# Performance work log

Hardware: AMD Instinct MI355X
Metric: run time of the kernel (lower is better)

## Reference

```python
import jax, jax.numpy as jnp
from jax import lax
import numpy as np

B, T, C_IN, H, W = 2, 4, 128, 64, 64
D_MODEL, N_Q, N_POINTS, PATCH, N_LAYERS = 256, 300, 8, 3, 6


def _sine_pos(Hh, Ww, d, temperature=10000.0):
    # mask is all-False, so cumsum of ones -> arange(1..H)/H * 2pi
    two_pi = 2.0 * np.pi
    yn = (jnp.arange(1, Hh + 1, dtype=jnp.float32) / (Hh + 1e-6)) * two_pi
    xn = (jnp.arange(1, Ww + 1, dtype=jnp.float32) / (Ww + 1e-6)) * two_pi
    q = d // 4
    i = jnp.arange(q, dtype=jnp.float32)
    dim_t = temperature ** (2.0 * jnp.floor(i / 2.0) / q)
    py = yn[:, None] / dim_t
    px = xn[:, None] / dim_t
    py = jnp.stack([jnp.sin(py), jnp.cos(py)], axis=-1).reshape(Hh, 2 * q)
    px = jnp.stack([jnp.sin(px), jnp.cos(px)], axis=-1).reshape(Ww, 2 * q)
    pos = jnp.concatenate([
        jnp.broadcast_to(py[:, None, :], (Hh, Ww, 2 * q)),
        jnp.broadcast_to(px[None, :, :], (Hh, Ww, 2 * q)),
    ], axis=-1)
    return jnp.transpose(pos, (2, 0, 1))  # [d,H,W]


def _sample_scale(fmap, ref, ps):
    # fmap [B,C,h,w]; ref [B,nQ,nP,2] in [0,1]. Bilinear grid_sample,
    # padding_mode='border', align_corners=True -> direct gather (no replication).
    Bc, C, h, w = fmap.shape
    half = (ps - 1) / 2.0
    off = jnp.linspace(-half, half, ps, dtype=jnp.float32)
    oy, ox = jnp.meshgrid(off, off, indexing='ij')  # [ps,ps]
    gx = ref[..., 0, None, None] * 2.0 - 1.0 + ox * (2.0 / w)  # [B,nQ,nP,ps,ps]
    gy = ref[..., 1, None, None] * 2.0 - 1.0 + oy * (2.0 / h)
    x = jnp.clip((gx + 1.0) * 0.5 * (w - 1), 0.0, w - 1.0)
    y = jnp.clip((gy + 1.0) * 0.5 * (h - 1), 0.0, h - 1.0)
    x0 = jnp.floor(x); y0 = jnp.floor(y)
    wx = x - x0; wy = y - y0
    x0i = x0.astype(jnp.int32); y0i = y0.astype(jnp.int32)
    x1i = jnp.minimum(x0i + 1, w - 1); y1i = jnp.minimum(y0i + 1, h - 1)

    def per_b(fb, y0b, x0b, y1b, x1b, wxb, wyb):
        v00 = fb[:, y0b, x0b]  # [C,nQ,nP,ps,ps]
        v01 = fb[:, y0b, x1b]
        v10 = fb[:, y1b, x0b]
        v11 = fb[:, y1b, x1b]
        return (v00 * (1 - wxb) * (1 - wyb) + v01 * wxb * (1 - wyb)
                + v10 * (1 - wxb) * wyb + v11 * wxb * wyb)

    out = jax.vmap(per_b)(fmap, y0i, x0i, y1i, x1i, wx, wy)  # [B,C,nQ,nP,ps,ps]
    return jnp.transpose(out, (0, 2, 3, 4, 5, 1))  # [B,nQ,nP,ps,ps,C]


def reference(feat, pred_boxes_init, w_tf, b_tf, w_in, b_in, w_lat, b_lat, w_sm, b_sm,
              q_embed, q_pos, Wq, bq, Wo, bo, Wp1, bp1, Wp2, bp2,
              w_r1, b_r1, w_r2, b_r2, w_b1, b_b1, w_b2, b_b2, w_cls, b_cls):
    Bb, Tt, Cin, Hh, Ww = feat.shape
    d = w_in.shape[0]
    nP = w_r2.shape[0] // 2
    ps = int(round((Wp1.shape[-1] // d) ** 0.5))
    # temporal fuse: Conv3d kernel (3,1,1), padding (1,0,0)
    x = lax.conv_general_dilated(jnp.transpose(feat, (0, 2, 1, 3, 4)), w_tf,
                                 (1, 1, 1), [(1, 1), (0, 0), (0, 0)],
                                 dimension_numbers=('NCDHW', 'OIDHW', 'NCDHW'))
    x = x + b_tf[None, :, None, None, None]
    x = x.mean(axis=2)  # [B,Cin,H,W]
    x = jnp.einsum('bchw,dc->bdhw', x, w_in) + b_in[None, :, None, None]
    x = x + _sine_pos(Hh, Ww, d)[None]
    # FPN over scales {1,2,4}: avg_pool -> 1x1 lateral -> 3x3 smooth
    feats = []
    for i, s in enumerate((1, 2, 4)):
        xi = x if s == 1 else x.reshape(Bb, d, Hh // s, s, Ww // s, s).mean(axis=(3, 5))
        xi = jnp.einsum('bchw,oc->bohw', xi, w_lat[i]) + b_lat[i][None, :, None, None]
        xi = lax.conv_general_dilated(xi, w_sm[i], (1, 1), [(1, 1), (1, 1)],
                                      dimension_numbers=('NCHW', 'OIHW', 'NCHW'))
        xi = xi + b_sm[i][None, :, None, None]
        feats.append(xi)
    nQ = q_embed.shape[0]
    queries = jnp.broadcast_to((q_embed + q_pos)[None], (Bb, nQ, d))
    boxes = pred_boxes_init
    inv_sqrt_d = 1.0 / float(np.sqrt(d))
    for l in range(Wq.shape[0]):
        h1 = jax.nn.relu(jnp.einsum('bqd,od->bqo', queries, w_r1) + b_r1)
        ro = jnp.tanh(jnp.einsum('bqd,od->bqo', h1, w_r2) + b_r2)
        ro = ro.reshape(Bb, nQ, nP, 2) * 0.5
        ref = jnp.clip(boxes[:, :, None, :2] + ro, 0.0, 1.0)
        sampled = jnp.concatenate([_sample_scale(f, ref, ps) for f in feats], axis=2)
        sampled = sampled[:, :, :nP]  # truncate multi-scale concat back to nP
        flat = sampled.reshape(Bb, nQ, nP, ps * ps * d)
        pv = jax.nn.relu(jnp.einsum('bqpi,oi->bqpo', flat, Wp1[l]) + bp1[l])
        pv = jnp.einsum('bqpd,od->bqpo', pv, Wp2[l]) + bp2[l]
        kv = pv.mean(axis=2)  # [B,nP_q,d] -> [B,nQ,d]
        q = jnp.einsum('bqd,od->bqo', queries, Wq[l]) + bq[l]
        attn = jax.nn.softmax(jnp.einsum('bqd,bkd->bqk', q, kv) * inv_sqrt_d, axis=-1)
        out = jnp.einsum('bqk,bkd->bqd', attn, kv)
        queries = queries + (jnp.einsum('bqd,od->bqo', out, Wo[l]) + bo[l])
        hb = jax.nn.relu(jnp.einsum('bqd,od->bqo', queries, w_b1) + b_b1)
        delta = jax.nn.sigmoid(jnp.einsum('bqd,od->bqo', hb, w_b2) + b_b2)
        boxes = jnp.clip(boxes + 0.1 * jnp.tanh(delta - 0.5), 0.0, 1.0)
    logits = (jnp.einsum('bqd,od->bqo', queries, w_cls) + b_cls)[..., 0]
    return logits, boxes


def setup_inputs() -> dict:
    key = jax.random.key(0)
    keys = iter(jax.random.split(key, 48))

    def nrm(shape, s=0.02):
        return jax.random.normal(next(keys), shape, dtype=jnp.float32) * s

    inp = {
        'feat': jax.random.normal(next(keys), (B, T, C_IN, H, W), dtype=jnp.float32),
        'pred_boxes_init': jax.random.uniform(next(keys), (B, N_Q, 4), dtype=jnp.float32),
        'w_tf': nrm((C_IN, C_IN, 3, 1, 1)), 'b_tf': jnp.zeros((C_IN,), jnp.float32),
        'w_in': nrm((D_MODEL, C_IN)), 'b_in': jnp.zeros((D_MODEL,), jnp.float32),
        'w_lat': nrm((3, D_MODEL, D_MODEL)), 'b_lat': jnp.zeros((3, D_MODEL), jnp.float32),
        'w_sm': nrm((3, D_MODEL, D_MODEL, 3, 3)), 'b_sm': jnp.zeros((3, D_MODEL), jnp.float32),
        'q_embed': nrm((N_Q, D_MODEL), 1.0), 'q_pos': nrm((N_Q, D_MODEL), 1.0),
        'Wq': nrm((N_LAYERS, D_MODEL, D_MODEL)), 'bq': jnp.zeros((N_LAYERS, D_MODEL), jnp.float32),
        'Wo': nrm((N_LAYERS, D_MODEL, D_MODEL)), 'bo': jnp.zeros((N_LAYERS, D_MODEL), jnp.float32),
        'Wp1': nrm((N_LAYERS, D_MODEL, PATCH * PATCH * D_MODEL)), 'bp1': jnp.zeros((N_LAYERS, D_MODEL), jnp.float32),
        'Wp2': nrm((N_LAYERS, D_MODEL, D_MODEL)), 'bp2': jnp.zeros((N_LAYERS, D_MODEL), jnp.float32),
        'w_r1': nrm((D_MODEL, D_MODEL)), 'b_r1': jnp.zeros((D_MODEL,), jnp.float32),
        'w_r2': nrm((2 * N_POINTS, D_MODEL)), 'b_r2': jnp.zeros((2 * N_POINTS,), jnp.float32),
        'w_b1': nrm((D_MODEL, D_MODEL)), 'b_b1': jnp.zeros((D_MODEL,), jnp.float32),
        'w_b2': nrm((4, D_MODEL)), 'b_b2': jnp.zeros((4,), jnp.float32),
        'w_cls': nrm((1, D_MODEL)), 'b_cls': jnp.zeros((1,), jnp.float32),
    }
    return inp
```

## Files before the change

### kernel.cpp

```cpp
#include <hip/hip_runtime.h>
#include <hip/hip_bf16.h>
#include <math.h>

#define BB 2
#define TT 4
#define CIN 128
#define DM 256
#define NQ 300
#define NP 8
#define PS 3
#define NL 6
#define HW 4096
#define KP 2304

typedef __attribute__((ext_vector_type(8))) short short8;
typedef __attribute__((ext_vector_type(4))) short short4_t;
typedef __attribute__((ext_vector_type(4))) float f32x4;
typedef unsigned short ushort_t;

static __device__ __forceinline__ ushort_t f2bf(float f) {
  __hip_bfloat16 h = __float2bfloat16(f);
  return *reinterpret_cast<ushort_t*>(&h);
}
static __device__ __forceinline__ float bf2f(ushort_t u) {
  return __uint_as_float(((unsigned)u) << 16);
}

__global__ void k_prep(const float* __restrict__ w_in, const float* __restrict__ w_lat,
                       const float* __restrict__ Wo, const float* __restrict__ w_b1,
                       const float* __restrict__ w_r1, const float* __restrict__ Wp1,
                       ushort_t* __restrict__ win_bf, ushort_t* __restrict__ wlat_bf,
                       ushort_t* __restrict__ wo_bf, ushort_t* __restrict__ wb1_bf,
                       ushort_t* __restrict__ wr1_bf, ushort_t* __restrict__ wp1_bf,
                       const float* __restrict__ w_tf, ushort_t* __restrict__ tct,
                       const float* __restrict__ w_sm, ushort_t* __restrict__ wsm_bf,
                       const float* __restrict__ Wp2, const float* __restrict__ Wq,
                       ushort_t* __restrict__ wp2t, ushort_t* __restrict__ wqT,
                       const float* __restrict__ bq, const float* __restrict__ bp2,
                       const float* __restrict__ bo,
                       float* __restrict__ bqt, float* __restrict__ bfuse,
                       uint4* __restrict__ x2p_zero,
                       const float* __restrict__ b_tf, const float* __restrict__ b_in,
                       float* __restrict__ bias_comb,
                       const float* __restrict__ qe, const float* __restrict__ qp,
                       const float* __restrict__ pb, float* __restrict__ queries,
                       ushort_t* __restrict__ qbf, float* __restrict__ boxes) {
  __shared__ float bt[128];
  int b = blockIdx.x, t = threadIdx.x;
  if (b < 4064) {
    int i = b * 256 + t;
    const float* s; ushort_t* d; int base;
    if (i < 8192)         { s = w_in;  d = win_bf;  base = 0; }
    else if (i < 24576)   { s = w_lat; d = wlat_bf; base = 8192; }
    else if (i < 122880)  { s = Wo;    d = wo_bf;   base = 24576; }
    else if (i < 139264)  { s = w_b1;  d = wb1_bf;  base = 122880; }
    else if (i < 155648)  { s = w_r1;  d = wr1_bf;  base = 139264; }
    else                  { s = Wp1;   d = wp1_bf;  base = 155648; }
    int j = i - base;
    float4 v = ((const float4*)s)[j];
    d[j * 4 + 0] = f2bf(v.x);
    d[j * 4 + 1] = f2bf(v.y);
    d[j * 4 + 2] = f2bf(v.z);
    d[j * 4 + 3] = f2bf(v.w);
  } else if (b < 4320) {
    int i = (b - 4064) * 256 + t;
    int k = i >> 7, c = i & 127;
    int u = k >> 7, ci = k & 127;
    const float* wp = w_tf + ((size_t)(c * 128 + ci)) * 3;
    float w0 = wp[0], w1 = wp[1], w2 = wp[2];
    float coef = (u == 0) ? (w0 + w1) : (u == 3) ? (w1 + w2) : (w0 + w1 + w2);
    tct[(size_t)k * 128 + c] = f2bf(0.25f * coef);
  } else if (b < 6624) {
    int i = (b - 4320) * 256 + t;
    int n = i / KP;
    int r = i - n * KP;
    int tp = r >> 8, c = r & 255;
    wsm_bf[i] = f2bf(w_sm[((size_t)(n * 256 + c)) * 9 + tp]);
  } else if (b < 9696) {
    int i = (b - 6624) * 256 + t;
    if (i < 393216) {
      int l = i >> 16, r = i & 65535;
      int d = r >> 8, o = r & 255;
      wp2t[i] = f2bf(Wp2[((size_t)(l * 256 + o)) * 256 + d]);
    } else {
      int j = i - 393216;
      int l = j >> 16, r = j & 65535;
      int c = r >> 8, o = r & 255;
      wqT[j] = f2bf(Wq[((size_t)(l * 256 + o)) * 256 + c]);
    }
  } else if (b < 9708) {
    int i = (b - 9696) * 256 + t;
    if (i < 1536) {
      int l = i >> 8, d = i & 255;
      float a = 0.f;
      for (int o = 0; o < 256; ++o)
        a += bq[l * 256 + o] * Wp2[((size_t)(l * 256 + o)) * 256 + d];
      bqt[i] = a;
    } else {
      int j = i - 1536;
      int l = j >> 8, o2 = j & 255;
      float a = bo[l * 256 + o2];
      for (int o = 0; o < 256; ++o)
        a += bp2[l * 256 + o] * Wo[((size_t)(l * 256 + o2)) * 256 + o];
      bfuse[j] = a;
    }
  } else if (b < 10797) {
    int j = (b - 9708) * 256 + t;
    if (j < 278784) x2p_zero[j] = make_uint4(0u, 0u, 0u, 0u);
  } else if (b < 10798) {
    int d = t;
    if (d < 128) bt[d] = b_tf[d];
    __syncthreads();
    float a = b_in[d];
    for (int c = 0; c < 128; ++c) a += w_in[d * 128 + c] * bt[c];
    bias_comb[d] = a;
  } else {
    int i = (b - 10798) * 256 + t;
    if (i < BB * NQ * DM) {
      int rd = i % (NQ * DM);
      float v = qe[rd] + qp[rd];
      queries[i] = v;
      qbf[i] = f2bf(v);
    }
    if (i < BB * NQ * 4) boxes[i] = pb[i];
  }
}

__global__ __launch_bounds__(256) void k_wcompose(const ushort_t* __restrict__ wp2t,
                                                  const ushort_t* __restrict__ wqT,
                                                  const ushort_t* __restrict__ wo_bf,
                                                  ushort_t* __restrict__ wqt,
                                                  ushort_t* __restrict__ wfuse) {
  __shared__ ushort_t As[64 * 36];
  __shared__ ushort_t Bs[64 * 36];
  int z = blockIdx.z, l = z % 6;
  const ushort_t* A;
  const ushort_t* W;
  ushort_t* C;
  if (z < 6) { A = wp2t + l * 65536; W = wqT + l * 65536; C = wqt + l * 65536; }
  else       { A = wo_bf + l * 65536; W = wp2t + l * 65536; C = wfuse + l * 65536; }
  int tid = threadIdx.x;
  int bm = blockIdx.x * 64, bn = blockIdx.y * 64;
  int w = tid >> 6, lane = tid & 63;
  int wm = (w & 1) * 32, wn = (w >> 1) * 32;
  int q = lane >> 4, ml = lane & 15;
  f32x4 acc[2][2] = {};
  int srow = tid >> 2, scol = (tid & 3) * 8;
  const ushort_t* Ag = A + (size_t)(bm + srow) * 256 + scol;
  const ushort_t* Wg = W + (size_t)(bn + srow) * 256 + scol;
  for (int k0 = 0; k0 < 256; k0 += 32) {
    short8 av = *(const short8*)(Ag + k0);
    short8 wv = *(const short8*)(Wg + k0);
    *(short8*)(As + srow * 36 + scol) = av;
    *(short8*)(Bs + srow * 36 + scol) = wv;
    __syncthreads();
    short8 a0 = *(const short8*)(As + (wm + ml) * 36 + q * 8);
    short8 a1 = *(const short8*)(As + (wm + 16 + ml) * 36 + q * 8);
    short8 b0 = *(const short8*)(Bs + (wn + ml) * 36 + q * 8);
    short8 b1 = *(const short8*)(Bs + (wn + 16 + ml) * 36 + q * 8);
    acc[0][0] = __builtin_amdgcn_mfma_f32_16x16x32_bf16(a0, b0, acc[0][0], 0, 0, 0);
    acc[0][1] = __builtin_amdgcn_mfma_f32_16x16x32_bf16(a0, b1, acc[0][1], 0, 0, 0);
    acc[1][0] = __builtin_amdgcn_mfma_f32_16x16x32_bf16(a1, b0, acc[1][0], 0, 0, 0);
    acc[1][1] = __builtin_amdgcn_mfma_f32_16x16x32_bf16(a1, b1, acc[1][1], 0, 0, 0);
    __syncthreads();
  }
#pragma unroll
  for (int i = 0; i < 2; ++i)
#pragma unroll
    for (int j = 0; j < 2; ++j) {
      int cn = bn + wn + j * 16 + ml;
#pragma unroll
      for (int r = 0; r < 4; ++r) {
        int rm = bm + wm + i * 16 + q * 4 + r;
        C[(size_t)rm * 256 + cn] = f2bf(acc[i][j][r]);
      }
    }
}

__global__ __launch_bounds__(256) void k_tr(const float* __restrict__ feat,
                                            ushort_t* __restrict__ featT) {
  __shared__ float ldsF[64][65];
  int tid = threadIdx.x;
  int gs = blockIdx.x;
  int b = gs >> 6;
  int s0 = (gs & 63) * 64;
  int k0 = blockIdx.y * 64;
  int kk = tid >> 2, sc0 = (tid & 3) * 16;
  {
    int k = k0 + kk;
    int u = k >> 7, ci = k & 127;
    const float* src = feat + (((size_t)(b * 4 + u) * 128 + ci) << 12) + s0 + sc0;
#pragma unroll
    for (int j = 0; j < 4; ++j) {
      float4 v = *(const float4*)(src + j * 4);
      ldsF[kk][sc0 + j * 4 + 0] = v.x;
      ldsF[kk][sc0 + j * 4 + 1] = v.y;
      ldsF[kk][sc0 + j * 4 + 2] = v.z;
      ldsF[kk][sc0 + j * 4 + 3] = v.w;
    }
  }
  __syncthreads();
#pragma unroll
  for (int p = 0; p < 2; ++p) {
    int idx = p * 256 + tid;
    int s_l = idx >> 3, kc = (idx & 7) * 8;
    short8 v;
#pragma unroll
    for (int j = 0; j < 8; ++j) v[j] = (short)f2bf(ldsF[kc + j][s_l]);
    *(short8*)(featT + (size_t)(b * 4096 + s0 + s_l) * 512 + k0 + kc) = v;
  }
}

__global__ __launch_bounds__(256) void k_feat2(const ushort_t* __restrict__ featT,
                                               const ushort_t* __restrict__ wcomb,
                                               const float* __restrict__ biasc,
                                               ushort_t* __restrict__ xcl) {
  __shared__ ushort_t As[32 * 36];
  __shared__ ushort_t Bs[64 * 36];
  __shared__ float dimt_s[256];
  int tid = threadIdx.x;
  {
    int dd = tid & 127;
    int ii = dd >> 1;
    dimt_s[tid] = powf(10000.0f, (2.0f * (float)(ii >> 1)) / 64.0f);
  }
  int bm = blockIdx.x * 32, bn = blockIdx.y * 64;
  int w = tid >> 6, lane = tid & 63;
  int wm = (w & 1) * 16, wn = (w >> 1) * 32;
  int q = lane >> 4, ml = lane & 15;
  int sra = tid >> 3, sca = (tid & 7) * 4;
  int srb = tid >> 2, scb = (tid & 3) * 8;
  const ushort_t* Ag = featT + (size_t)(bm + sra) * 512 + sca;
  const ushort_t* Wg = wcomb + (size_t)(bn + srb) * 512 + scb;
  f32x4 acc[2] = {};
  short4_t av = *(const short4_t*)Ag;
  short8 wv = *(const short8*)Wg;
  for (int k0 = 0; k0 < 512; k0 += 32) {
    *(short4_t*)(As + sra * 36 + sca) = av;
    *(short8*)(Bs + srb * 36 + scb) = wv;
    __syncthreads();
    if (k0 + 32 < 512) {
      av = *(const short4_t*)(Ag + k0 + 32);
      wv = *(const short8*)(Wg + k0 + 32);
    }
    short8 a = *(const short8*)(As + (wm + ml) * 36 + q * 8);
    short8 b0 = *(const short8*)(Bs + (wn + ml) * 36 + q * 8);
    short8 b1 = *(const short8*)(Bs + (wn + 16 + ml) * 36 + q * 8);
    acc[0] = __builtin_amdgcn_mfma_f32_16x16x32_bf16(a, b0, acc[0], 0, 0, 0);
    acc[1] = __builtin_amdgcn_mfma_f32_16x16x32_bf16(a, b1, acc[1], 0, 0, 0);
    __syncthreads();
  }
  const float FKT = 6.28318530717958647692f / 64.000001f;
#pragma unroll
  for (int j = 0; j < 2; ++j) {
    int cn = bn + wn + j * 16 + ml;
    float dimt = dimt_s[cn];
    float bC = biasc[cn];
    bool isx = cn >= 128;
    bool isc = cn & 1;
#pragma unroll
    for (int r = 0; r < 4; ++r) {
      int rm = bm + wm + q * 4 + r;
      int s = rm & 4095;
      int y = s >> 6, x = s & 63;
      float ang = (float)((isx ? x : y) + 1) * FKT / dimt;
      float pos = isc ? cosf(ang) : sinf(ang);
      xcl[(size_t)rm * 256 + cn] = f2bf(acc[j][r] + bC + pos);
    }
  }
}

template <int ACT, int OUTMODE, int MG>
__global__ __launch_bounds__(256) void k_gemm_bf16(const ushort_t* __restrict__ A,
                                                   const ushort_t* __restrict__ W,
                                                   const float* __restrict__ bias,
                                                   const float* __restrict__ res,
                                                   float* __restrict__ Cf,
                                                   ushort_t* __restrict__ Cb,
                                                   int M, int N, int K,
                                                   const ushort_t* __restrict__ W2,
                                                   const float* __restrict__ bias2,
                                                   const ushort_t* __restrict__ W3,
                                                   const float* __restrict__ bias3) {
  __shared__ ushort_t As[64 * 36];
  __shared__ ushort_t Bs[64 * 36];
  int tid = threadIdx.x;
  int bm = blockIdx.x * 64, bn = blockIdx.y * 64;
  int w = tid >> 6, lane = tid & 63;
  int wm = (w & 1) * 32, wn = (w >> 1) * 32;
  int q = lane >> 4, ml = lane & 15;
  f32x4 acc[2][2] = {};
  int srow = tid >> 2, scol = (tid & 3) * 8;
  int ga = bm + srow;
  if (MG) ga = min(ga, M - 1);
  const ushort_t* Ag = A + (size_t)ga * K + scol;
  const ushort_t* Wg;
  if (OUTMODE == 7) {
    int seg = bn >> 8;
    const ushort_t* Wb = (seg == 0) ? W : ((seg == 1) ? W2 : W3);
    Wg = Wb + (size_t)((bn & 255) + srow) * K + scol;
  } else if (OUTMODE == 4) {
    const ushort_t* Wb = (bn < 256) ? W : W2;
    Wg = Wb + (size_t)((bn & 255) + srow) * K + scol;
  } else {
    Wg = W + (size_t)(bn + srow) * K + scol;
  }
  for (int k0 = 0; k0 < K; k0 += 32) {
    short8 av = *(const short8*)(Ag + k0);
    short8 wv = *(const short8*)(Wg + k0);
    *(short8*)(As + srow * 36 + scol) = av;
    *(short8*)(Bs + srow * 36 + scol) = wv;
    __syncthreads();
    short8 a0 = *(const short8*)(As + (wm + ml) * 36 + q * 8);
    short8 a1 = *(const short8*)(As + (wm + 16 + ml) * 36 + q * 8);
    short8 b0 = *(const short8*)(Bs + (wn + ml) * 36 + q * 8);
    short8 b1 = *(const short8*)(Bs + (wn + 16 + ml) * 36 + q * 8);
    acc[0][0] = __builtin_amdgcn_mfma_f32_16x16x32_bf16(a0, b0, acc[0][0], 0, 0, 0);
    acc[0][1] = __builtin_amdgcn_mfma_f32_16x16x32_bf16(a0, b1, acc[0][1], 0, 0, 0);
    acc[1][0] = __builtin_amdgcn_mfma_f32_16x16x32_bf16(a1, b0, acc[1][0], 0, 0, 0);
    acc[1][1] = __builtin_amdgcn_mfma_f32_16x16x32_bf16(a1, b1, acc[1][1], 0, 0, 0);
    __syncthreads();
  }
#pragma unroll
  for (int i = 0; i < 2; ++i) {
#pragma unroll
    for (int j = 0; j < 2; ++j) {
      int cn = bn + wn + j * 16 + ml;
      float bsv;
      if (OUTMODE == 7) {
        int seg = cn >> 8;
        bsv = ((seg == 0) ? bias : ((seg == 1) ? bias2 : bias3))[cn & 255];
      } else if (OUTMODE == 4) {
        bsv = ((cn < 256) ? bias : bias2)[cn & 255];
      } else {
        bsv = bias ? bias[cn] : 0.f;
      }
#pragma unroll
      for (int r = 0; r < 4; ++r) {
        int rm = bm + wm + i * 16 + q * 4 + r;
        if (MG && rm >= M) continue;
        float v = acc[i][j][r] + bsv;
        if (OUTMODE == 0) {
          if (ACT == 1) v = fmaxf(v, 0.f);
          Cf[(size_t)rm * N + cn] = v;
        } else if (OUTMODE == 1) {
          int b = rm >> 12, rem = rm & 4095;
          int y = rem >> 6, xx = rem & 63;
          Cb[(((size_t)(b * 66 + y + 1)) * 66 + xx + 1) * 256 + cn] = f2bf(v);
        } else if (OUTMODE == 2) {
          v += res[(size_t)rm * N + cn];
          Cf[(size_t)rm * N + cn] = v;
          Cb[(size_t)rm * N + cn] = f2bf(v);
        } else if (OUTMODE == 4) {
          if (cn < 256) Cf[(size_t)rm * 256 + cn] = fmaxf(v, 0.f);
          else Cb[(size_t)rm * 256 + (cn & 255)] = f2bf(v);
        } else if (OUTMODE == 6) {
          Cb[(size_t)rm * N + cn] = f2bf(v);
        } else if (OUTMODE == 7) {
          if (cn < 256) Cf[(size_t)rm * 256 + cn] = fmaxf(v, 0.f);
          else if (cn < 512) ((float*)Cb)[(size_t)rm * 256 + (cn & 255)] = fmaxf(v, 0.f);
          else ((ushort_t*)res)[(size_t)rm * 256 + (cn & 255)] = f2bf(v);
        }
      }
    }
  }
}

__global__ __launch_bounds__(256) void k_wp1_split(const ushort_t* __restrict__ A,
                                                   const ushort_t* __restrict__ W,
                                                   ushort_t* __restrict__ part) {
  __shared__ ushort_t As[64 * 36];
  __shared__ ushort_t Bs[64 * 36];
  int tid = threadIdx.x;
  int bm = blockIdx.x * 64, bn = blockIdx.y * 64;
  int kz = blockIdx.z * 768;
  int w = tid >> 6, lane = tid & 63;
  int wm = (w & 1) * 32, wn = (w >> 1) * 32;
  int q = lane >> 4, ml = lane & 15;
  int srow = tid >> 2, scol = (tid & 3) * 8;
  const ushort_t* Ag = A + (size_t)(bm + srow) * KP + kz + scol;
  const ushort_t* Wg = W + (size_t)(bn + srow) * KP + kz + scol;
  f32x4 acc[2][2] = {};
  short8 av = *(const short8*)(Ag);
  short8 wv = *(const short8*)(Wg);
  for (int k0 = 0; k0 < 768; k0 += 32) {
    *(short8*)(As + srow * 36 + scol) = av;
    *(short8*)(Bs + srow * 36 + scol) = wv;
    __syncthreads();
    if (k0 + 32 < 768) {
      av = *(const short8*)(Ag + k0 + 32);
      wv = *(const short8*)(Wg + k0 + 32);
    }
    short8 a0 = *(const short8*)(As + (wm + ml) * 36 + q * 8);
    short8 a1 = *(const short8*)(As + (wm + 16 + ml) * 36 + q * 8);
    short8 b0 = *(const short8*)(Bs + (wn + ml) * 36 + q * 8);
    short8 b1 = *(const short8*)(Bs + (wn + 16 + ml) * 36 + q * 8);
    acc[0][0] = __builtin_amdgcn_mfma_f32_16x16x32_bf16(a0, b0, acc[0][0], 0, 0, 0);
    acc[0][1] = __builtin_amdgcn_mfma_f32_16x16x32_bf16(a0, b1, acc[0][1], 0, 0, 0);
    acc[1][0] = __builtin_amdgcn_mfma_f32_16x16x32_bf16(a1, b0, acc[1][0], 0, 0, 0);
    acc[1][1] = __builtin_amdgcn_mfma_f32_16x16x32_bf16(a1, b1, acc[1][1], 0, 0, 0);
    __syncthreads();
  }
  ushort_t* pz = part + (size_t)blockIdx.z * 4800 * 256;
#pragma unroll
  for (int i = 0; i < 2; ++i)
#pragma unroll
    for (int j = 0; j < 2; ++j) {
      int cn = bn + wn + j * 16 + ml;
#pragma unroll
      for (int r = 0; r < 4; ++r) {
        int rm = bm + wm + i * 16 + q * 4 + r;
        pz[(size_t)rm * 256 + cn] = f2bf(acc[i][j][r]);
      }
    }
}

__global__ __launch_bounds__(256) void k_wp1_reduce(const ushort_t* __restrict__ part,
                                                    const float* __restrict__ bias,
                                                    ushort_t* __restrict__ pvm) {
  int row = blockIdx.x;
  int d = threadIdx.x;
  float b = bias[d];
  float s = 0.f;
#pragma unroll
  for (int p = 0; p < 8; ++p) {
    size_t idx = (size_t)(row * 8 + p) * 256 + d;
    float v = bf2f(part[idx]) + bf2f(part[idx + (size_t)4800 * 256]) +
              bf2f(part[idx + (size_t)2 * 4800 * 256]) + b;
    s += fmaxf(v, 0.f);
  }
  pvm[(size_t)row * 256 + d] = f2bf(s * 0.125f);
}

__global__ __launch_bounds__(256) void k_conv3(const ushort_t* __restrict__ x2p,
                                               const ushort_t* __restrict__ wsm,
                                               const float* __restrict__ bsm,
                                               ushort_t* __restrict__ fcl) {
  __shared__ ushort_t As[32 * 36];
  __shared__ ushort_t Bs[64 * 36];
  int tid = threadIdx.x;
  int bm = blockIdx.x * 32, bn = blockIdx.y * 64;
  int w = tid >> 6, lane = tid & 63;
  int wm = (w & 1) * 16, wn = (w >> 1) * 32;
  int q = lane >> 4, ml = lane & 15;
  int sra = tid >> 3, sca = (tid & 7) * 4;
  int srb = tid >> 2, scb = (tid & 3) * 8;
  int sA = bm + sra;
  int b = sA >> 12, rem = sA & 4095;
  size_t pbase = ((size_t)(b * 66 + (rem >> 6)) * 66 + (rem & 63)) * 256;
  const ushort_t* Wg = wsm + (size_t)(bn + srb) * KP + scb;
  auto loadA = [&](int k0) {
    int ka = k0 + sca;
    int t9 = ka >> 8;
    int ky = t9 / 3, kx = t9 - ky * 3;
    return *(const short4_t*)(x2p + pbase + (size_t)(ky * 66 + kx) * 256 + (ka & 255));
  };
  f32x4 acc[2] = {};
  short4_t av = loadA(0);
  short8 wv = *(const short8*)(Wg);
  for (int k0 = 0; k0 < KP; k0 += 32) {
    *(short4_t*)(As + sra * 36 + sca) = av;
    *(short8*)(Bs + srb * 36 + scb) = wv;
    __syncthreads();
    if (k0 + 32 < KP) {
      av = loadA(k0 + 32);
      wv = *(const short8*)(Wg + k0 + 32);
    }
    short8 a = *(const short8*)(As + (wm + ml) * 36 + q * 8);
    short8 b0 = *(const short8*)(Bs + (wn + ml) * 36 + q * 8);
    short8 b1 = *(const short8*)(Bs + (wn + 16 + ml) * 36 + q * 8);
    acc[0] = __builtin_amdgcn_mfma_f32_16x16x32_bf16(a, b0, acc[0], 0, 0, 0);
    acc[1] = __builtin_amdgcn_mfma_f32_16x16x32_bf16(a, b1, acc[1], 0, 0, 0);
    __syncthreads();
  }
#pragma unroll
  for (int j = 0; j < 2; ++j) {
    int cn = bn + wn + j * 16 + ml;
    float bsv = bsm[cn];
#pragma unroll
    for (int r = 0; r < 4; ++r) {
      int rm = bm + wm + q * 4 + r;
      fcl[(size_t)rm * 256 + cn] = f2bf(acc[j][r] + bsv);
    }
  }
}

__global__ __launch_bounds__(256) void k_sample(const ushort_t* __restrict__ fcl,
                                                const float* __restrict__ h1,
                                                const float* __restrict__ w_r2,
                                                const float* __restrict__ b_r2,
                                                const float* __restrict__ boxes,
                                                ushort_t* __restrict__ flat) {
  __shared__ float pr[8];
  __shared__ float bc2[2];
  int blk = blockIdx.x;
  int row = blk >> 3, p = blk & 7;
  int b = row / NQ;
  int tid = threadIdx.x;
  float h = h1[(size_t)row * 256 + tid];
  float px = h * w_r2[(size_t)(2 * p) * 256 + tid];
  float py = h * w_r2[(size_t)(2 * p + 1) * 256 + tid];
#pragma unroll
  for (int s = 32; s > 0; s >>= 1) {
    px += __shfl_down(px, s, 64);
    py += __shfl_down(py, s, 64);
  }
  int w = tid >> 6, lane = tid & 63;
  if (lane == 0) { pr[w * 2] = px; pr[w * 2 + 1] = py; }
  __syncthreads();
  if (tid == 0) {
    float sx = pr[0] + pr[2] + pr[4] + pr[6] + b_r2[2 * p];
    float sy = pr[1] + pr[3] + pr[5] + pr[7] + b_r2[2 * p + 1];
    float rx = boxes[row * 4 + 0] + 0.5f * tanhf(sx);
    float ry = boxes[row * 4 + 1] + 0.5f * tanhf(sy);
    bc2[0] = fminf(fmaxf(rx, 0.f), 1.f);
    bc2[1] = fminf(fmaxf(ry, 0.f), 1.f);
  }
  __syncthreads();
  float rx = bc2[0], ry = bc2[1];
  int c = tid;
  const ushort_t* fb = fcl + (size_t)b * HW * DM;
  ushort_t* op = flat + (size_t)blk * KP;
#pragma unroll
  for (int jy = 0; jy < 3; ++jy) {
    float yy = (ry + (float)(jy - 1) * (1.0f / 64.0f)) * 63.0f;
    yy = fminf(fmaxf(yy, 0.f), 63.0f);
    float y0f = floorf(yy);
    float wy = yy - y0f;
    int y0 = (int)y0f;
    int y1 = min(y0 + 1, 63);
#pragma unroll
    for (int jx = 0; jx < 3; ++jx) {
      float xx = (rx + (float)(jx - 1) * (1.0f / 64.0f)) * 63.0f;
      xx = fminf(fmaxf(xx, 0.f), 63.0f);
      float x0f = floorf(xx);
      float wx = xx - x0f;
      int x0 = (int)x0f;
      int x1 = min(x0 + 1, 63);
      float v00 = bf2f(fb[(y0 * 64 + x0) * DM + c]);
      float v01 = bf2f(fb[(y0 * 64 + x1) * DM + c]);
      float v10 = bf2f(fb[(y1 * 64 + x0) * DM + c]);
      float v11 = bf2f(fb[(y1 * 64 + x1) * DM + c]);
      float v = v00 * (1.f - wx) * (1.f - wy) + v01 * wx * (1.f - wy) +
                v10 * (1.f - wx) * wy + v11 * wx * wy;
      op[(jy * 3 + jx) * DM + c] = f2bf(v);
    }
  }
}

__global__ __launch_bounds__(256) void k_attn(const ushort_t* __restrict__ qt,
                                              const ushort_t* __restrict__ pvm,
                                              ushort_t* __restrict__ ctx) {
  __shared__ float qs[256];
  __shared__ float sc[512];
  __shared__ float red[256];
  int row = blockIdx.x;
  int b = row / NQ;
  int tid = threadIdx.x;
  qs[tid] = bf2f(qt[(size_t)row * DM + tid]);
  __syncthreads();
  const ushort_t* kvB = pvm + (size_t)b * NQ * DM;
#pragma unroll
  for (int s2 = 0; s2 < 2; ++s2) {
    int k = tid + s2 * 256;
    float v = -1e30f;
    if (k < NQ) {
      const ushort_t* kp = kvB + (size_t)k * DM;
      float a = 0.f;
#pragma unroll
      for (int d = 0; d < 256; d += 8) {
        short8 k8 = *(const short8*)(kp + d);
        const float* qd = qs + d;
        a += bf2f((ushort_t)k8[0]) * qd[0];
        a += bf2f((ushort_t)k8[1]) * qd[1];
        a += bf2f((ushort_t)k8[2]) * qd[2];
        a += bf2f((ushort_t)k8[3]) * qd[3];
        a += bf2f((ushort_t)k8[4]) * qd[4];
        a += bf2f((ushort_t)k8[5]) * qd[5];
        a += bf2f((ushort_t)k8[6]) * qd[6];
        a += bf2f((ushort_t)k8[7]) * qd[7];
      }
      v = a * (1.0f / 16.0f);
    }
    sc[k] = v;
  }
  __syncthreads();
  red[tid] = fmaxf(sc[tid], sc[tid + 256]);
  __syncthreads();
  for (int st = 128; st > 0; st >>= 1) {
    if (tid < st) red[tid] = fmaxf(red[tid], red[tid + st]);
    __syncthreads();
  }
  float mx = red[0];
  __syncthreads();
  float e0 = (tid < NQ) ? expf(sc[tid] - mx) : 0.f;
  float e1 = (tid + 256 < NQ) ? expf(sc[tid + 256] - mx) : 0.f;
  sc[tid] = e0;
  sc[tid + 256] = e1;
  red[tid] = e0 + e1;
  __syncthreads();
  for (int st = 128; st > 0; st >>= 1) {
    if (tid < st) red[tid] += red[tid + st];
    __syncthreads();
  }
  float inv = 1.0f / red[0];
  __syncthreads();
  float acc = 0.f;
#pragma unroll 4
  for (int k = 0; k < NQ; ++k)
    acc += sc[k] * bf2f(kvB[(size_t)k * DM + tid]);
  ctx[(size_t)row * DM + tid] = f2bf(acc * inv);
}

__global__ __launch_bounds__(256) void k_boxf(const float* __restrict__ hb,
                                              const float* __restrict__ w_b2,
                                              const float* __restrict__ b_b2,
                                              float* __restrict__ boxes,
                                              int last,
                                              const float* __restrict__ queries,
                                              const float* __restrict__ w_cls,
                                              const float* __restrict__ b_cls,
                                              float* __restrict__ out) {
  __shared__ float nb[4];
  int row = blockIdx.x;
  int tid = threadIdx.x;
  int j = tid >> 6, lane = tid & 63;
  float4 hv = *(const float4*)(hb + (size_t)row * 256 + lane * 4);
  float4 wv = *(const float4*)(w_b2 + (size_t)j * 256 + lane * 4);
  float aa = hv.x * wv.x + hv.y * wv.y + hv.z * wv.z + hv.w * wv.w;
#pragma unroll
  for (int s = 32; s > 0; s >>= 1) aa += __shfl_down(aa, s, 64);
  if (lane == 0) {
    aa += b_b2[j];
    float delta = 1.0f / (1.0f + expf(-aa));
    float v = boxes[row * 4 + j] + 0.1f * tanhf(delta - 0.5f);
    v = fminf(fmaxf(v, 0.f), 1.f);
    boxes[row * 4 + j] = v;
    nb[j] = v;
  }
  if (last) {
    __syncthreads();
    if (j == 0) {
      float4 qv = *(const float4*)(queries + (size_t)row * 256 + lane * 4);
      float4 cv = *(const float4*)(w_cls + lane * 4);
      float a2 = qv.x * cv.x + qv.y * cv.y + qv.z * cv.z + qv.w * cv.w;
#pragma unroll
      for (int s = 32; s > 0; s >>= 1) a2 += __shfl_down(a2, s, 64);
      if (lane == 0) out[row] = a2 + b_cls[0];
    } else if (j == 1 && lane < 4) {
      out[600 + row * 4 + lane] = nb[lane];
    }
  }
}

extern "C" void kernel_launch(void* const* d_in, const int* in_sizes, int n_in,
                              void* d_out, int out_size, void* d_ws, size_t ws_size,
                              hipStream_t stream) {
  const float* feat   = (const float*)d_in[0];
  const float* pb     = (const float*)d_in[1];
  const float* w_tf   = (const float*)d_in[2];
  const float* b_tf   = (const float*)d_in[3];
  const float* w_in   = (const float*)d_in[4];
  const float* b_in   = (const float*)d_in[5];
  const float* w_lat  = (const float*)d_in[6];
  const float* b_lat  = (const float*)d_in[7];
  const float* w_sm   = (const float*)d_in[8];
  const float* b_sm   = (const float*)d_in[9];
  const float* q_embed= (const float*)d_in[10];
  const float* q_pos  = (const float*)d_in[11];
  const float* Wq     = (const float*)d_in[12];
  const float* bq     = (const float*)d_in[13];
  const float* Wo     = (const float*)d_in[14];
  const float* bo     = (const float*)d_in[15];
  const float* Wp1    = (const float*)d_in[16];
  const float* bp1    = (const float*)d_in[17];
  const float* Wp2    = (const float*)d_in[18];
  const float* bp2    = (const float*)d_in[19];
  const float* w_r1   = (const float*)d_in[20];
  const float* b_r1   = (const float*)d_in[21];
  const float* w_r2   = (const float*)d_in[22];
  const float* b_r2   = (const float*)d_in[23];
  const float* w_b1   = (const float*)d_in[24];
  const float* b_b1   = (const float*)d_in[25];
  const float* w_b2   = (const float*)d_in[26];
  const float* b_b2   = (const float*)d_in[27];
  const float* w_cls  = (const float*)d_in[28];
  const float* b_cls  = (const float*)d_in[29];
  float* out = (float*)d_out;

  float* ws = (float*)d_ws;
  size_t off = 0;
  auto alloc = [&](size_t n) { float* p = ws + off; off += n; return p; };
  ushort_t* flat    = (ushort_t*)alloc(5529600);
  ushort_t* part    = (ushort_t*)alloc(1843200);
  ushort_t* featT   = (ushort_t*)alloc(2097152);
  ushort_t* xcl     = (ushort_t*)alloc(1048576);
  ushort_t* x2p     = (ushort_t*)alloc(1115136);
  ushort_t* fcl     = (ushort_t*)alloc(1048576);
  ushort_t* wcomb   = (ushort_t*)alloc(65536);
  ushort_t* tct     = (ushort_t*)alloc(32768);
  ushort_t* win_bf  = (ushort_t*)alloc(16384);
  float*    biasc   = alloc(256);
  ushort_t* wlat_bf = (ushort_t*)alloc(32768);
  ushort_t* wsm_bf  = (ushort_t*)alloc(294912);
  ushort_t* wp1_bf  = (ushort_t*)alloc(1769472);
  ushort_t* wo_bf   = (ushort_t*)alloc(196608);
  ushort_t* wb1_bf  = (ushort_t*)alloc(32768);
  ushort_t* wr1_bf  = (ushort_t*)alloc(32768);
  ushort_t* wp2t    = (ushort_t*)alloc(196608);
  ushort_t* wqT     = (ushort_t*)alloc(196608);
  ushort_t* wqt_bf  = (ushort_t*)alloc(196608);
  ushort_t* wfuse_bf= (ushort_t*)alloc(196608);
  float*    bqt     = alloc(1536);
  float*    bfuse   = alloc(1536);
  float* queries = alloc(153600);
  ushort_t* qbf  = (ushort_t*)alloc(76800);
  float* h1      = alloc(153600);
  ushort_t* qt   = (ushort_t*)alloc(76800);
  ushort_t* ctx  = (ushort_t*)alloc(76800);
  float* hb      = alloc(153600);
  ushort_t* pvm  = (ushort_t*)alloc(76800);
  float* boxes   = alloc(2400);
  (void)ws_size; (void)in_sizes; (void)n_in; (void)out_size;

  k_prep<<<11398, 256, 0, stream>>>(w_in, w_lat, Wo, w_b1, w_r1, Wp1,
                                    win_bf, wlat_bf, wo_bf, wb1_bf, wr1_bf, wp1_bf,
                                    w_tf, tct, w_sm, wsm_bf,
                                    Wp2, Wq, wp2t, wqT,
                                    bq, bp2, bo, bqt, bfuse,
                                    (uint4*)x2p, b_tf, b_in, biasc,
                                    q_embed, q_pos, pb, queries, qbf, boxes);
  k_gemm_bf16<0, 6, 0><<<dim3(4, 8), 256, 0, stream>>>(win_bf, tct, nullptr, nullptr,
                                                       nullptr, wcomb, 256, 512, 128,
                                                       nullptr, nullptr, nullptr, nullptr);
  k_wcompose<<<dim3(4, 4, 12), 256, 0, stream>>>(wp2t, wqT, wo_bf, wqt_bf, wfuse_bf);

  k_tr<<<dim3(128, 8), 256, 0, stream>>>(feat, featT);
  k_feat2<<<dim3(256, 4), 256, 0, stream>>>(featT, wcomb, biasc, xcl);
  k_gemm_bf16<0, 1, 0><<<dim3(128, 4), 256, 0, stream>>>(xcl, wlat_bf, b_lat, nullptr,
                                                         nullptr, x2p, BB * HW, 256, 256,
                                                         nullptr, nullptr, nullptr, nullptr);
  k_conv3<<<dim3(256, 4), 256, 0, stream>>>(x2p, wsm_bf, b_sm, fcl);

  const int M6 = BB * NQ;
  const int Mp = BB * NQ * NP;
  dim3 g600((M6 + 63) / 64, 4);
  dim3 g600w((M6 + 63) / 64, 8);
  dim3 g600m((M6 + 63) / 64, 12);
  dim3 gsk(Mp / 64, 4, 3);

  k_gemm_bf16<0, 4, 1><<<g600w, 256, 0, stream>>>(qbf, wr1_bf, b_r1, nullptr, h1,
                                                  qt, M6, 512, 256,
                                                  wqt_bf, bqt, nullptr, nullptr);
  for (int l = 0; l < NL; ++l) {
    k_sample<<<Mp, 256, 0, stream>>>(fcl, h1, w_r2, b_r2, boxes, flat);
    k_wp1_split<<<gsk, 256, 0, stream>>>(flat, wp1_bf + (size_t)l * 256 * KP, part);
    k_wp1_reduce<<<600, 256, 0, stream>>>(part, bp1 + (size_t)l * DM, pvm);
    k_attn<<<M6, 256, 0, stream>>>(qt, pvm, ctx);
    k_gemm_bf16<0, 2, 1><<<g600, 256, 0, stream>>>(ctx, wfuse_bf + (size_t)l * 65536,
                                                   bfuse + l * 256, queries, queries,
                                                   qbf, M6, DM, DM,
                                                   nullptr, nullptr, nullptr, nullptr);
    int ln = (l + 1) % NL;
    k_gemm_bf16<0, 7, 1><<<g600m, 256, 0, stream>>>(qbf, wb1_bf, b_b1, (const float*)qt,
                                                    hb, (ushort_t*)h1, M6, 768, 256,
                                                    wr1_bf, b_r1,
                                                    wqt_bf + (size_t)ln * 65536,
                                                    bqt + ln * 256);
    k_boxf<<<M6, 256, 0, stream>>>(hb, w_b2, b_b2, boxes, (l == NL - 1) ? 1 : 0,
                                   queries, w_cls, b_cls, out);
  }
}
```

Baseline: 728.9 us.

## Fuse output projection into attention and box update into sampling kernel

Moves the fused Wo·Wp2 projection plus residual into the attention kernel, which removes the ctx buffer and one GEMM launch per layer. The box-refinement head is folded into the next layer's sampling kernel using ping-pong box buffers, so k_boxf runs only once at the end. Weight composition now reads fp32 weights directly, with an on-the-fly transpose and bf16 conversion, instead of using separately prepped transposed copies, and the GEMM loop gains register prefetch of the next K tile. The per-row projection in k_attn is a scalar dot product per block, which may be less efficient than the MFMA GEMM it replaces, and the box head is recomputed redundantly by every point block.

```diff
diff --git a/kernel.cpp b/kernel.cpp
--- a/kernel.cpp
+++ b/kernel.cpp
@@ -27,15 +27,14 @@
 }
 
 __global__ void k_prep(const float* __restrict__ w_in, const float* __restrict__ w_lat,
-                       const float* __restrict__ Wo, const float* __restrict__ w_b1,
+                       const float* __restrict__ w_b1,
                        const float* __restrict__ w_r1, const float* __restrict__ Wp1,
                        ushort_t* __restrict__ win_bf, ushort_t* __restrict__ wlat_bf,
-                       ushort_t* __restrict__ wo_bf, ushort_t* __restrict__ wb1_bf,
+                       ushort_t* __restrict__ wb1_bf,
                        ushort_t* __restrict__ wr1_bf, ushort_t* __restrict__ wp1_bf,
                        const float* __restrict__ w_tf, ushort_t* __restrict__ tct,
                        const float* __restrict__ w_sm, ushort_t* __restrict__ wsm_bf,
-                       const float* __restrict__ Wp2, const float* __restrict__ Wq,
-                       ushort_t* __restrict__ wp2t, ushort_t* __restrict__ wqT,
+                       const float* __restrict__ Wp2, const float* __restrict__ Wo,
                        const float* __restrict__ bq, const float* __restrict__ bp2,
                        const float* __restrict__ bo,
                        float* __restrict__ bqt, float* __restrict__ bfuse,
@@ -47,49 +46,36 @@
                        ushort_t* __restrict__ qbf, float* __restrict__ boxes) {
   __shared__ float bt[128];
   int b = blockIdx.x, t = threadIdx.x;
-  if (b < 4064) {
+  if (b < 3680) {
     int i = b * 256 + t;
     const float* s; ushort_t* d; int base;
     if (i < 8192)         { s = w_in;  d = win_bf;  base = 0; }
     else if (i < 24576)   { s = w_lat; d = wlat_bf; base = 8192; }
-    else if (i < 122880)  { s = Wo;    d = wo_bf;   base = 24576; }
-    else if (i < 139264)  { s = w_b1;  d = wb1_bf;  base = 122880; }
-    else if (i < 155648)  { s = w_r1;  d = wr1_bf;  base = 139264; }
-    else                  { s = Wp1;   d = wp1_bf;  base = 155648; }
+    else if (i < 40960)   { s = w_b1;  d = wb1_bf;  base = 24576; }
+    else if (i < 57344)   { s = w_r1;  d = wr1_bf;  base = 40960; }
+    else                  { s = Wp1;   d = wp1_bf;  base = 57344; }
     int j = i - base;
     float4 v = ((const float4*)s)[j];
     d[j * 4 + 0] = f2bf(v.x);
     d[j * 4 + 1] = f2bf(v.y);
     d[j * 4 + 2] = f2bf(v.z);
     d[j * 4 + 3] = f2bf(v.w);
-  } else if (b < 4320) {
-    int i = (b - 4064) * 256 + t;
+  } else if (b < 3936) {
+    int i = (b - 3680) * 256 + t;
     int k = i >> 7, c = i & 127;
     int u = k >> 7, ci = k & 127;
     const float* wp = w_tf + ((size_t)(c * 128 + ci)) * 3;
     float w0 = wp[0], w1 = wp[1], w2 = wp[2];
     float coef = (u == 0) ? (w0 + w1) : (u == 3) ? (w1 + w2) : (w0 + w1 + w2);
     tct[(size_t)k * 128 + c] = f2bf(0.25f * coef);
-  } else if (b < 6624) {
-    int i = (b - 4320) * 256 + t;
+  } else if (b < 6240) {
+    int i = (b - 3936) * 256 + t;
     int n = i / KP;
     int r = i - n * KP;
     int tp = r >> 8, c = r & 255;
     wsm_bf[i] = f2bf(w_sm[((size_t)(n * 256 + c)) * 9 + tp]);
-  } else if (b < 9696) {
-    int i = (b - 6624) * 256 + t;
-    if (i < 393216) {
-      int l = i >> 16, r = i & 65535;
-      int d = r >> 8, o = r & 255;
-      wp2t[i] = f2bf(Wp2[((size_t)(l * 256 + o)) * 256 + d]);
-    } else {
-      int j = i - 393216;
-      int l = j >> 16, r = j & 65535;
-      int c = r >> 8, o = r & 255;
-      wqT[j] = f2bf(Wq[((size_t)(l * 256 + o)) * 256 + c]);
-    }
-  } else if (b < 9708) {
-    int i = (b - 9696) * 256 + t;
+  } else if (b < 6252) {
+    int i = (b - 6240) * 256 + t;
     if (i < 1536) {
       int l = i >> 8, d = i & 255;
       float a = 0.f;
@@ -104,10 +90,10 @@
         a += bp2[l * 256 + o] * Wo[((size_t)(l * 256 + o2)) * 256 + o];
       bfuse[j] = a;
     }
-  } else if (b < 10797) {
-    int j = (b - 9708) * 256 + t;
+  } else if (b < 7341) {
+    int j = (b - 6252) * 256 + t;
     if (j < 278784) x2p_zero[j] = make_uint4(0u, 0u, 0u, 0u);
-  } else if (b < 10798) {
+  } else if (b < 7342) {
     int d = t;
     if (d < 128) bt[d] = b_tf[d];
     __syncthreads();
@@ -115,7 +101,7 @@
     for (int c = 0; c < 128; ++c) a += w_in[d * 128 + c] * bt[c];
     bias_comb[d] = a;
   } else {
-    int i = (b - 10798) * 256 + t;
+    int i = (b - 7342) * 256 + t;
     if (i < BB * NQ * DM) {
       int rd = i % (NQ * DM);
       float v = qe[rd] + qp[rd];
@@ -126,33 +112,57 @@
   }
 }
 
-__global__ __launch_bounds__(256) void k_wcompose(const ushort_t* __restrict__ wp2t,
-                                                  const ushort_t* __restrict__ wqT,
-                                                  const ushort_t* __restrict__ wo_bf,
+__global__ __launch_bounds__(256) void k_wcompose(const float* __restrict__ Wp2,
+                                                  const float* __restrict__ Wq,
+                                                  const float* __restrict__ Wo,
                                                   ushort_t* __restrict__ wqt,
-                                                  ushort_t* __restrict__ wfuse) {
+                                                  ushort_t* __restrict__ wfuseT) {
   __shared__ ushort_t As[64 * 36];
   __shared__ ushort_t Bs[64 * 36];
   int z = blockIdx.z, l = z % 6;
-  const ushort_t* A;
-  const ushort_t* W;
-  ushort_t* C;
-  if (z < 6) { A = wp2t + l * 65536; W = wqT + l * 65536; C = wqt + l * 65536; }
-  else       { A = wo_bf + l * 65536; W = wp2t + l * 65536; C = wfuse + l * 65536; }
+  const float* Asrc = Wp2 + (size_t)l * 65536;
+  const float* Bsrc = ((z < 6) ? Wq : Wo) + (size_t)l * 65536;
+  ushort_t* C = ((z < 6) ? wqt : wfuseT) + (size_t)l * 65536;
+  bool btr = (z < 6);
   int tid = threadIdx.x;
   int bm = blockIdx.x * 64, bn = blockIdx.y * 64;
   int w = tid >> 6, lane = tid & 63;
   int wm = (w & 1) * 32, wn = (w >> 1) * 32;
   int q = lane >> 4, ml = lane & 15;
   f32x4 acc[2][2] = {};
-  int srow = tid >> 2, scol = (tid & 3) * 8;
-  const ushort_t* Ag = A + (size_t)(bm + srow) * 256 + scol;
-  const ushort_t* Wg = W + (size_t)(bn + srow) * 256 + scol;
+  int oo = tid >> 3, mg = (tid & 7) * 8;
+  int nr = tid >> 2, kg = (tid & 3) * 8;
   for (int k0 = 0; k0 < 256; k0 += 32) {
-    short8 av = *(const short8*)(Ag + k0);
-    short8 wv = *(const short8*)(Wg + k0);
-    *(short8*)(As + srow * 36 + scol) = av;
-    *(short8*)(Bs + srow * 36 + scol) = wv;
+    {
+      const float* sp = Asrc + (size_t)(k0 + oo) * 256 + bm + mg;
+      float4 f0 = *(const float4*)sp;
+      float4 f1 = *(const float4*)(sp + 4);
+      ushort_t* dst = As + oo;
+      dst[(mg + 0) * 36] = f2bf(f0.x); dst[(mg + 1) * 36] = f2bf(f0.y);
+      dst[(mg + 2) * 36] = f2bf(f0.z); dst[(mg + 3) * 36] = f2bf(f0.w);
+      dst[(mg + 4) * 36] = f2bf(f1.x); dst[(mg + 5) * 36] = f2bf(f1.y);
+      dst[(mg + 6) * 36] = f2bf(f1.z); dst[(mg + 7) * 36] = f2bf(f1.w);
+    }
+    if (btr) {
+      const float* sp = Bsrc + (size_t)(k0 + oo) * 256 + bn + mg;
+      float4 f0 = *(const float4*)sp;
+      float4 f1 = *(const float4*)(sp + 4);
+      ushort_t* dst = Bs + oo;
+      dst[(mg + 0) * 36] = f2bf(f0.x); dst[(mg + 1) * 36] = f2bf(f0.y);
+      dst[(mg + 2) * 36] = f2bf(f0.z); dst[(mg + 3) * 36] = f2bf(f0.w);
+      dst[(mg + 4) * 36] = f2bf(f1.x); dst[(mg + 5) * 36] = f2bf(f1.y);
+      dst[(mg + 6) * 36] = f2bf(f1.z); dst[(mg + 7) * 36] = f2bf(f1.w);
+    } else {
+      const float* sp = Bsrc + (size_t)(bn + nr) * 256 + k0 + kg;
+      float4 f0 = *(const float4*)sp;
+      float4 f1 = *(const float4*)(sp + 4);
+      short8 v;
+      v[0] = (short)f2bf(f0.x); v[1] = (short)f2bf(f0.y);
+      v[2] = (short)f2bf(f0.z); v[3] = (short)f2bf(f0.w);
+      v[4] = (short)f2bf(f1.x); v[5] = (short)f2bf(f1.y);
+      v[6] = (short)f2bf(f1.z); v[7] = (short)f2bf(f1.w);
+      *(short8*)(Bs + nr * 36 + kg) = v;
+    }
     __syncthreads();
     short8 a0 = *(const short8*)(As + (wm + ml) * 36 + q * 8);
     short8 a1 = *(const short8*)(As + (wm + 16 + ml) * 36 + q * 8);
@@ -305,12 +315,16 @@
   } else {
     Wg = W + (size_t)(bn + srow) * K + scol;
   }
+  short8 av = *(const short8*)(Ag);
+  short8 wv = *(const short8*)(Wg);
   for (int k0 = 0; k0 < K; k0 += 32) {
-    short8 av = *(const short8*)(Ag + k0);
-    short8 wv = *(const short8*)(Wg + k0);
     *(short8*)(As + srow * 36 + scol) = av;
     *(short8*)(Bs + srow * 36 + scol) = wv;
     __syncthreads();
+    if (k0 + 32 < K) {
+      av = *(const short8*)(Ag + k0 + 32);
+      wv = *(const short8*)(Wg + k0 + 32);
+    }
     short8 a0 = *(const short8*)(As + (wm + ml) * 36 + q * 8);
     short8 a1 = *(const short8*)(As + (wm + 16 + ml) * 36 + q * 8);
     short8 b0 = *(const short8*)(Bs + (wn + ml) * 36 + q * 8);
@@ -347,10 +361,6 @@
           int b = rm >> 12, rem = rm & 4095;
           int y = rem >> 6, xx = rem & 63;
           Cb[(((size_t)(b * 66 + y + 1)) * 66 + xx + 1) * 256 + cn] = f2bf(v);
-        } else if (OUTMODE == 2) {
-          v += res[(size_t)rm * N + cn];
-          Cf[(size_t)rm * N + cn] = v;
-          Cb[(size_t)rm * N + cn] = f2bf(v);
         } else if (OUTMODE == 4) {
           if (cn < 256) Cf[(size_t)rm * 256 + cn] = fmaxf(v, 0.f);
           else Cb[(size_t)rm * 256 + (cn & 255)] = f2bf(v);
@@ -489,14 +499,37 @@
                                                 const float* __restrict__ h1,
                                                 const float* __restrict__ w_r2,
                                                 const float* __restrict__ b_r2,
-                                                const float* __restrict__ boxes,
+                                                const float* __restrict__ boxesIn,
+                                                float* __restrict__ boxesOut,
+                                                const float* __restrict__ hb,
+                                                const float* __restrict__ w_b2,
+                                                const float* __restrict__ b_b2,
                                                 ushort_t* __restrict__ flat) {
   __shared__ float pr[8];
   __shared__ float bc2[2];
+  __shared__ float nb2[2];
   int blk = blockIdx.x;
   int row = blk >> 3, p = blk & 7;
   int b = row / NQ;
   int tid = threadIdx.x;
+  int w = tid >> 6, lane = tid & 63;
+  if (hb) {
+    float4 hv = *(const float4*)(hb + (size_t)row * 256 + lane * 4);
+    float4 wv = *(const float4*)(w_b2 + (size_t)w * 256 + lane * 4);
+    float aa = hv.x * wv.x + hv.y * wv.y + hv.z * wv.z + hv.w * wv.w;
+#pragma unroll
+    for (int s = 32; s > 0; s >>= 1) aa += __shfl_down(aa, s, 64);
+    if (lane == 0) {
+      aa += b_b2[w];
+      float delta = 1.0f / (1.0f + expf(-aa));
+      float v = boxesIn[row * 4 + w] + 0.1f * tanhf(delta - 0.5f);
+      v = fminf(fmaxf(v, 0.f), 1.f);
+      if (w < 2) nb2[w] = v;
+      if (p == 0) boxesOut[row * 4 + w] = v;
+    }
+  } else if (tid < 2) {
+    nb2[tid] = boxesIn[row * 4 + tid];
+  }
   float h = h1[(size_t)row * 256 + tid];
   float px = h * w_r2[(size_t)(2 * p) * 256 + tid];
   float py = h * w_r2[(size_t)(2 * p + 1) * 256 + tid];
@@ -505,14 +538,13 @@
     px += __shfl_down(px, s, 64);
     py += __shfl_down(py, s, 64);
   }
-  int w = tid >> 6, lane = tid & 63;
   if (lane == 0) { pr[w * 2] = px; pr[w * 2 + 1] = py; }
   __syncthreads();
   if (tid == 0) {
     float sx = pr[0] + pr[2] + pr[4] + pr[6] + b_r2[2 * p];
     float sy = pr[1] + pr[3] + pr[5] + pr[7] + b_r2[2 * p + 1];
-    float rx = boxes[row * 4 + 0] + 0.5f * tanhf(sx);
-    float ry = boxes[row * 4 + 1] + 0.5f * tanhf(sy);
+    float rx = nb2[0] + 0.5f * tanhf(sx);
+    float ry = nb2[1] + 0.5f * tanhf(sy);
     bc2[0] = fminf(fmaxf(rx, 0.f), 1.f);
     bc2[1] = fminf(fmaxf(ry, 0.f), 1.f);
   }
@@ -550,10 +582,14 @@
 
 __global__ __launch_bounds__(256) void k_attn(const ushort_t* __restrict__ qt,
                                               const ushort_t* __restrict__ pvm,
-                                              ushort_t* __restrict__ ctx) {
+                                              const ushort_t* __restrict__ wfT,
+                                              const float* __restrict__ bfuse_l,
+                                              float* __restrict__ queries,
+                                              ushort_t* __restrict__ qbf) {
   __shared__ float qs[256];
   __shared__ float sc[512];
   __shared__ float red[256];
+  __shared__ float pr4[1024];
   int row = blockIdx.x;
   int b = row / NQ;
   int tid = threadIdx.x;
@@ -609,7 +645,27 @@
 #pragma unroll 4
   for (int k = 0; k < NQ; ++k)
     acc += sc[k] * bf2f(kvB[(size_t)k * DM + tid]);
-  ctx[(size_t)row * DM + tid] = f2bf(acc * inv);
+  qs[tid] = acc * inv;
+  __syncthreads();
+  int oq = (tid & 63) * 4, dq = (tid >> 6) * 64;
+  float a0 = 0.f, a1 = 0.f, a2 = 0.f, a3 = 0.f;
+  const ushort_t* wp = wfT + (size_t)dq * 256 + oq;
+#pragma unroll 8
+  for (int dd = 0; dd < 64; ++dd) {
+    float cc = qs[dq + dd];
+    short4_t wv = *(const short4_t*)(wp + (size_t)dd * 256);
+    a0 += cc * bf2f((ushort_t)wv[0]);
+    a1 += cc * bf2f((ushort_t)wv[1]);
+    a2 += cc * bf2f((ushort_t)wv[2]);
+    a3 += cc * bf2f((ushort_t)wv[3]);
+  }
+  float* pb4 = pr4 + (tid >> 6) * 256 + oq;
+  pb4[0] = a0; pb4[1] = a1; pb4[2] = a2; pb4[3] = a3;
+  __syncthreads();
+  float v = pr4[tid] + pr4[256 + tid] + pr4[512 + tid] + pr4[768 + tid] +
+            bfuse_l[tid] + queries[(size_t)row * DM + tid];
+  queries[(size_t)row * DM + tid] = v;
+  qbf[(size_t)row * DM + tid] = f2bf(v);
 }
 
 __global__ __launch_bounds__(256) void k_boxf(const float* __restrict__ hb,
@@ -704,36 +760,32 @@
   ushort_t* wlat_bf = (ushort_t*)alloc(32768);
   ushort_t* wsm_bf  = (ushort_t*)alloc(294912);
   ushort_t* wp1_bf  = (ushort_t*)alloc(1769472);
-  ushort_t* wo_bf   = (ushort_t*)alloc(196608);
   ushort_t* wb1_bf  = (ushort_t*)alloc(32768);
   ushort_t* wr1_bf  = (ushort_t*)alloc(32768);
-  ushort_t* wp2t    = (ushort_t*)alloc(196608);
-  ushort_t* wqT     = (ushort_t*)alloc(196608);
   ushort_t* wqt_bf  = (ushort_t*)alloc(196608);
-  ushort_t* wfuse_bf= (ushort_t*)alloc(196608);
+  ushort_t* wfuseT  = (ushort_t*)alloc(196608);
   float*    bqt     = alloc(1536);
   float*    bfuse   = alloc(1536);
   float* queries = alloc(153600);
   ushort_t* qbf  = (ushort_t*)alloc(76800);
   float* h1      = alloc(153600);
   ushort_t* qt   = (ushort_t*)alloc(76800);
-  ushort_t* ctx  = (ushort_t*)alloc(76800);
   float* hb      = alloc(153600);
   ushort_t* pvm  = (ushort_t*)alloc(76800);
-  float* boxes   = alloc(2400);
+  float* boxesA  = alloc(2400);
+  float* boxesB  = alloc(2400);
   (void)ws_size; (void)in_sizes; (void)n_in; (void)out_size;
 
-  k_prep<<<11398, 256, 0, stream>>>(w_in, w_lat, Wo, w_b1, w_r1, Wp1,
-                                    win_bf, wlat_bf, wo_bf, wb1_bf, wr1_bf, wp1_bf,
-                                    w_tf, tct, w_sm, wsm_bf,
-                                    Wp2, Wq, wp2t, wqT,
-                                    bq, bp2, bo, bqt, bfuse,
-                                    (uint4*)x2p, b_tf, b_in, biasc,
-                                    q_embed, q_pos, pb, queries, qbf, boxes);
+  k_prep<<<7942, 256, 0, stream>>>(w_in, w_lat, w_b1, w_r1, Wp1,
+                                   win_bf, wlat_bf, wb1_bf, wr1_bf, wp1_bf,
+                                   w_tf, tct, w_sm, wsm_bf,
+                                   Wp2, Wo, bq, bp2, bo, bqt, bfuse,
+                                   (uint4*)x2p, b_tf, b_in, biasc,
+                                   q_embed, q_pos, pb, queries, qbf, boxesA);
   k_gemm_bf16<0, 6, 0><<<dim3(4, 8), 256, 0, stream>>>(win_bf, tct, nullptr, nullptr,
                                                        nullptr, wcomb, 256, 512, 128,
                                                        nullptr, nullptr, nullptr, nullptr);
-  k_wcompose<<<dim3(4, 4, 12), 256, 0, stream>>>(wp2t, wqT, wo_bf, wqt_bf, wfuse_bf);
+  k_wcompose<<<dim3(4, 4, 12), 256, 0, stream>>>(Wp2, Wq, Wo, wqt_bf, wfuseT);
 
   k_tr<<<dim3(128, 8), 256, 0, stream>>>(feat, featT);
   k_feat2<<<dim3(256, 4), 256, 0, stream>>>(featT, wcomb, biasc, xcl);
@@ -744,7 +796,6 @@
 
   const int M6 = BB * NQ;
   const int Mp = BB * NQ * NP;
-  dim3 g600((M6 + 63) / 64, 4);
   dim3 g600w((M6 + 63) / 64, 8);
   dim3 g600m((M6 + 63) / 64, 12);
   dim3 gsk(Mp / 64, 4, 3);
@@ -752,22 +803,24 @@
   k_gemm_bf16<0, 4, 1><<<g600w, 256, 0, stream>>>(qbf, wr1_bf, b_r1, nullptr, h1,
                                                   qt, M6, 512, 256,
                                                   wqt_bf, bqt, nullptr, nullptr);
+  float* bcur = boxesA;
+  float* bnext = boxesB;
   for (int l = 0; l < NL; ++l) {
-    k_sample<<<Mp, 256, 0, stream>>>(fcl, h1, w_r2, b_r2, boxes, flat);
+    const float* hbp = (l == 0) ? nullptr : hb;
+    k_sample<<<Mp, 256, 0, stream>>>(fcl, h1, w_r2, b_r2, bcur, bnext,
+                                     hbp, w_b2, b_b2, flat);
+    if (l > 0) { float* tmp = bcur; bcur = bnext; bnext = tmp; }
     k_wp1_split<<<gsk, 256, 0, stream>>>(flat, wp1_bf + (size_t)l * 256 * KP, part);
     k_wp1_reduce<<<600, 256, 0, stream>>>(part, bp1 + (size_t)l * DM, pvm);
-    k_attn<<<M6, 256, 0, stream>>>(qt, pvm, ctx);
-    k_gemm_bf16<0, 2, 1><<<g600, 256, 0, stream>>>(ctx, wfuse_bf + (size_t)l * 65536,
-                                                   bfuse + l * 256, queries, queries,
-                                                   qbf, M6, DM, DM,
-                                                   nullptr, nullptr, nullptr, nullptr);
+    k_attn<<<M6, 256, 0, stream>>>(qt, pvm, wfuseT + (size_t)l * 65536,
+                                   bfuse + l * 256, queries, qbf);
     int ln = (l + 1) % NL;
     k_gemm_bf16<0, 7, 1><<<g600m, 256, 0, stream>>>(qbf, wb1_bf, b_b1, (const float*)qt,
                                                     hb, (ushort_t*)h1, M6, 768, 256,
                                                     wr1_bf, b_r1,
                                                     wqt_bf + (size_t)ln * 65536,
                                                     bqt + ln * 256);
-    k_boxf<<<M6, 256, 0, stream>>>(hb, w_b2, b_b2, boxes, (l == NL - 1) ? 1 : 0,
-                                   queries, w_cls, b_cls, out);
-  }
-}
+  }
+  k_boxf<<<M6, 256, 0, stream>>>(hb, w_b2, b_b2, bcur, 1,
+                                 queries, w_cls, b_cls, out);
+}
```

Result: faster. 697.2 us (-4.4%).
